# Performance work log

Measured on AMD Instinct MI355X. Metric: run time of the kernel, lower is better.

Reference implementation:

```python
import jax, jax.numpy as jnp
import numpy as np

E = 8       # n_experts
K = 2       # k_experts
D_IN = 1024
D_OUT = 1024
D_EXP = 2048
N = 16384   # tokens (batch*seq, forward requires 2D input)


def setup_inputs() -> dict:
    key = jax.random.key(0)
    ks = jax.random.split(key, 4)
    x = jax.random.normal(ks[0], (N, D_IN), jnp.float32)
    Wg = jax.random.normal(ks[1], (E, D_IN), jnp.float32) * 0.02      # router weight
    bg = jnp.zeros((E,), jnp.float32)                                  # router bias
    W_in = jax.random.normal(ks[2], (E, D_EXP, D_IN), jnp.float32) * 0.02
    b_in = jnp.zeros((E, D_EXP), jnp.float32)                          # w_in_bias_init=0.0
    W_out = jax.random.normal(ks[3], (E, D_OUT, D_EXP), jnp.float32) * 0.02  # bias=False
    return {"x": x, "Wg": Wg, "bg": bg, "W_in": W_in, "b_in": b_in, "W_out": W_out}


def moe_forward(x, Wg, bg, W_in, b_in, W_out):
    # Eval mode: gate jitter / solu jitter / dropouts are training-only no-ops.
    n = x.shape[0]
    # --- routing ---
    logits = x @ Wg.T + bg                                 # [N, E]
    probs = jax.nn.softmax(logits, axis=-1)
    mean_probs = probs.mean(axis=0)                        # [E]
    k_vals, k_idx = jax.lax.top_k(probs, K)                # [N, K]
    k_w = k_vals / k_vals.sum(axis=-1, keepdims=True)      # renormalized gate weights
    counts = jnp.bincount(k_idx.reshape(-1), length=E)     # [E] int
    load_balancing_loss = E * jnp.sum((counts.astype(x.dtype) / n) * mean_probs)
    # --- dispatch + expert w_in (loop over fixed small E; combine with one-hot mask) ---
    sel = jax.nn.one_hot(k_idx, E, dtype=x.dtype)          # [N, K, E]
    h = jnp.zeros((n, K, D_EXP), x.dtype)                  # preacts per (token, slot)
    for e in range(E):
        he = x @ W_in[e].T + b_in[e]                       # [N, D_EXP]
        h = h + sel[:, :, e][..., None] * he[:, None, :]
    # --- SoLU (eval): softmax(preacts) * preacts over hidden dim ---
    acts = jax.nn.softmax(h, axis=-1) * h                  # [N, K, D_EXP]
    # --- expert w_out (no bias) ---
    out = jnp.zeros((n, K, D_OUT), x.dtype)
    for e in range(E):
        oe = jnp.einsum('nkh,oh->nko', acts, W_out[e])
        out = out + sel[:, :, e][..., None] * oe
    # --- weighted combine over the K chosen experts ---
    outputs = (out * k_w[..., None]).sum(axis=1)           # [N, D_OUT]
    return outputs, load_balancing_loss


def reference(x, Wg, bg, W_in, b_in, W_out):
    return moe_forward(x, Wg, bg, W_in, b_in, W_out)
```

## Files before the change

### kernel.cpp

```cpp
#include <hip/hip_runtime.h>
#include <hip/hip_bf16.h>
#include <stdint.h>

#define E_EXP 8
#define NTOK  16384
#define DIN   1024
#define DEXP  2048
#define DOUT  1024
#define NSLOT (NTOK*2)
#define MAXT  264

typedef __attribute__((ext_vector_type(8))) short short8;
typedef __attribute__((ext_vector_type(8))) unsigned short ushort8;
typedef __attribute__((ext_vector_type(4))) unsigned short ushort4v;
typedef __attribute__((ext_vector_type(4))) float f32x4;

__device__ __forceinline__ unsigned short f2bf(float f){
  union { float f; uint32_t u; } v; v.f = f;
  uint32_t r = (v.u + 0x7FFFu + ((v.u >> 16) & 1u)) >> 16;
  return (unsigned short)r;
}
__device__ __forceinline__ float bf2f(unsigned short u){
  union { uint32_t u; float f; } v; v.u = ((uint32_t)u) << 16;
  return v.f;
}

__device__ __forceinline__ void async16(const void* g, void* l){
  __builtin_amdgcn_global_load_lds(
      (const __attribute__((address_space(1))) void*)g,
      (__attribute__((address_space(3))) void*)l, 16, 0, 0);
}

#define VMCNT6() asm volatile("s_waitcnt vmcnt(6)" ::: "memory")
#define VMCNT0() asm volatile("s_waitcnt vmcnt(0)" ::: "memory")
#define BARRIER() do { asm volatile("" ::: "memory"); __builtin_amdgcn_s_barrier(); asm volatile("" ::: "memory"); } while(0)

__global__ __launch_bounds__(256) void cast_bf16(const float* __restrict__ s,
                                                 unsigned short* __restrict__ d, int n){
  int i = (blockIdx.x*256 + threadIdx.x)*8;
  if (i >= n) return;
  float4 a = *(const float4*)(s+i);
  float4 b = *(const float4*)(s+i+4);
  ushort8 o;
  o[0]=f2bf(a.x); o[1]=f2bf(a.y); o[2]=f2bf(a.z); o[3]=f2bf(a.w);
  o[4]=f2bf(b.x); o[5]=f2bf(b.y); o[6]=f2bf(b.z); o[7]=f2bf(b.w);
  *(ushort8*)(d+i) = o;
}

__global__ __launch_bounds__(256) void router(
    const float* __restrict__ x, const float* __restrict__ Wg, const float* __restrict__ bg,
    unsigned short* __restrict__ xb,
    int* __restrict__ eidx, float* __restrict__ gw,
    int* __restrict__ counts, float* __restrict__ probsum)
{
  __shared__ float sWg[E_EXP*DIN];
  __shared__ float sps[E_EXP];
  __shared__ int   scnt[E_EXP];
  const int tid = threadIdx.x;
  for (int i = tid; i < E_EXP*DIN; i += 256) sWg[i] = Wg[i];
  if (tid < E_EXP){ sps[tid]=0.f; scnt[tid]=0; }
  __syncthreads();
  const int lane = tid & 63;
  const int wv   = tid >> 6;
  for (int it = 0; it < 16; ++it){
    const int token = blockIdx.x*64 + wv*16 + it;
    float4 xv[4];
#pragma unroll
    for (int j=0;j<4;++j) xv[j] = *(const float4*)&x[(size_t)token*DIN + j*256 + lane*4];
#pragma unroll
    for (int j=0;j<4;++j){
      ushort4v o;
      o[0]=f2bf(xv[j].x); o[1]=f2bf(xv[j].y); o[2]=f2bf(xv[j].z); o[3]=f2bf(xv[j].w);
      *(ushort4v*)&xb[(size_t)token*DIN + j*256 + lane*4] = o;
    }
    float p[E_EXP];
#pragma unroll
    for (int e2=0;e2<E_EXP;++e2){
      float s = 0.f;
#pragma unroll
      for (int j=0;j<4;++j){
        const float4 w4 = *(const float4*)&sWg[e2*DIN + j*256 + lane*4];
        s += xv[j].x*w4.x + xv[j].y*w4.y + xv[j].z*w4.z + xv[j].w*w4.w;
      }
      p[e2] = s;
    }
#pragma unroll
    for (int d=1; d<64; d<<=1){
#pragma unroll
      for (int e2=0;e2<E_EXP;++e2) p[e2] += __shfl_xor(p[e2], d);
    }
    if (lane == 0){
      float mx = -1e30f;
#pragma unroll
      for (int e2=0;e2<E_EXP;++e2){ p[e2] += bg[e2]; mx = fmaxf(mx, p[e2]); }
      float se = 0.f;
#pragma unroll
      for (int e2=0;e2<E_EXP;++e2){ p[e2] = __expf(p[e2]-mx); se += p[e2]; }
      const float inv = 1.f/se;
#pragma unroll
      for (int e2=0;e2<E_EXP;++e2){ p[e2] *= inv; atomicAdd(&sps[e2], p[e2]); }
      int i1 = 0;
#pragma unroll
      for (int e2=1;e2<E_EXP;++e2) if (p[e2] > p[i1]) i1 = e2;
      int i2 = (i1==0) ? 1 : 0;
#pragma unroll
      for (int e2=0;e2<E_EXP;++e2) if (e2 != i1 && p[e2] > p[i2]) i2 = e2;
      const float v1 = p[i1], v2 = p[i2], s12 = v1 + v2;
      eidx[2*token]   = i1; eidx[2*token+1] = i2;
      gw[2*token]     = v1/s12; gw[2*token+1] = v2/s12;
      atomicAdd(&scnt[i1], 1); atomicAdd(&scnt[i2], 1);
    }
  }
  __syncthreads();
  if (tid < E_EXP){ atomicAdd(&counts[tid], scnt[tid]); atomicAdd(&probsum[tid], sps[tid]); }
}

__global__ void finalize(const int* __restrict__ counts, const float* __restrict__ probsum,
                         float* __restrict__ loss_out, int* __restrict__ offs,
                         int* __restrict__ cursor, int* __restrict__ tile_e,
                         int* __restrict__ tile_row, int* __restrict__ ntiles)
{
  if (threadIdx.x != 0 || blockIdx.x != 0) return;
  int off = 0, nt = 0;
  float loss = 0.f;
  offs[0] = 0;
  for (int e2=0;e2<E_EXP;++e2){
    const int c = counts[e2];
    loss += (float)c * probsum[e2];
    cursor[e2] = 0;
    const int t = (c + 127) >> 7;
    for (int i=0;i<t;++i){ tile_e[nt] = e2; tile_row[nt] = off + i*128; ++nt; }
    off += c;
    offs[e2+1] = off;
  }
  *ntiles = nt;
  *loss_out = loss * (8.f/((float)NTOK*(float)NTOK));
}

__global__ __launch_bounds__(256) void scatter(const int* __restrict__ eidx,
    const int* __restrict__ offs, int* __restrict__ cursor,
    int* __restrict__ ptok, int* __restrict__ inv)
{
  const int t = blockIdx.x*256 + threadIdx.x;
  if (t >= NTOK) return;
#pragma unroll
  for (int s=0;s<2;++s){
    const int e2  = eidx[2*t+s];
    const int pos = offs[e2] + atomicAdd(&cursor[e2], 1);
    ptok[pos] = t;
    inv[2*t+s] = pos;
  }
}

__global__ __launch_bounds__(512, 2) void gemm1(
    const unsigned short* __restrict__ xb,
    const unsigned short* __restrict__ wib,
    const float* __restrict__ b_in,
    unsigned short* __restrict__ H,
    const int* __restrict__ ptok,
    const int* __restrict__ offs,
    const int* __restrict__ tile_e,
    const int* __restrict__ tile_row,
    const int* __restrict__ ntiles)
{
  if ((int)blockIdx.y >= *ntiles) return;
  const int e    = tile_e[blockIdx.y];
  const int row0 = tile_row[blockIdx.y];
  const int seg_end = offs[e+1];
  const int col0 = blockIdx.x * 256;

  __shared__ unsigned short As[2][128*64];
  __shared__ unsigned short Bs[2][256*64];

  const int tid  = threadIdx.x;
  const int lane = tid & 63;
  const int wv   = tid >> 6;
  const int wm   = wv >> 2;
  const int wn   = wv & 3;
  const int srow = tid >> 3;
  const int scol = ((tid & 7) ^ (srow & 7)) * 8;

  const unsigned short* ag[2];
#pragma unroll
  for (int i = 0; i < 2; ++i){
    int g = row0 + i*64 + srow; if (g > NSLOT-1) g = NSLOT-1;
    const int tok = ptok[g];
    ag[i] = xb + (size_t)tok*DIN + scol;
  }
  const unsigned short* bg4[4];
#pragma unroll
  for (int i = 0; i < 4; ++i)
    bg4[i] = wib + ((size_t)e*DEXP + col0 + i*64 + srow)*DIN + scol;
  float bias[4];
#pragma unroll
  for (int n = 0; n < 4; ++n)
    bias[n] = b_in[e*DEXP + col0 + wn*64 + n*16 + (lane&15)];

  f32x4 acc[4][4] = {};
  const int NK = DIN/64;
  int cur = 0;

#pragma unroll
  for (int i = 0; i < 2; ++i) async16(ag[i],  &As[0][(i*64 + wv*8)*64]);
#pragma unroll
  for (int i = 0; i < 4; ++i) async16(bg4[i], &Bs[0][(i*64 + wv*8)*64]);

#pragma unroll 2
  for (int kt = 0; kt < NK; ++kt){
    BARRIER();
    if (kt + 1 < NK){
      const int ko = (kt+1)*64;
#pragma unroll
      for (int i = 0; i < 2; ++i) async16(ag[i]  + ko, &As[cur^1][(i*64 + wv*8)*64]);
#pragma unroll
      for (int i = 0; i < 4; ++i) async16(bg4[i] + ko, &Bs[cur^1][(i*64 + wv*8)*64]);
      VMCNT6();
    } else {
      VMCNT0();
    }
    BARRIER();

    __builtin_amdgcn_s_setprio(1);
#pragma unroll
    for (int kk = 0; kk < 2; ++kk){
      const int ksl = ((kk*4 + (lane>>4)) ^ (lane & 7)) * 8;
      short8 a[4], b[4];
#pragma unroll
      for (int m = 0; m < 4; ++m)
        a[m] = *(const short8*)&As[cur][(wm*64 + m*16 + (lane&15))*64 + ksl];
#pragma unroll
      for (int n = 0; n < 4; ++n)
        b[n] = *(const short8*)&Bs[cur][(wn*64 + n*16 + (lane&15))*64 + ksl];
#pragma unroll
      for (int m = 0; m < 4; ++m)
#pragma unroll
        for (int n = 0; n < 4; ++n)
          acc[m][n] = __builtin_amdgcn_mfma_f32_16x16x32_bf16(a[m], b[n], acc[m][n], 0, 0, 0);
    }
    __builtin_amdgcn_s_setprio(0);
    cur ^= 1;
  }

#pragma unroll
  for (int m = 0; m < 4; ++m){
#pragma unroll
    for (int j = 0; j < 4; ++j){
      const int r = wm*64 + m*16 + (lane>>4)*4 + j;
      const int g = row0 + r;
      if (g < seg_end){
#pragma unroll
        for (int n = 0; n < 4; ++n){
          const int c = col0 + wn*64 + n*16 + (lane&15);
          H[(size_t)g*DEXP + c] = f2bf(acc[m][n][j] + bias[n]);
        }
      }
    }
  }
}

__global__ __launch_bounds__(256) void solu(unsigned short* __restrict__ H){
  const size_t row = blockIdx.x;
  unsigned short* hp = H + row*DEXP;
  const int tid  = threadIdx.x;
  const int lane = tid & 63;
  const int wv   = tid >> 6;
  const short8 hv = *(const short8*)&hp[tid*8];
  float f[8];
#pragma unroll
  for (int j=0;j<8;++j) f[j] = bf2f((unsigned short)hv[j]);
  float mx = f[0];
#pragma unroll
  for (int j=1;j<8;++j) mx = fmaxf(mx, f[j]);
  for (int d=1; d<64; d<<=1) mx = fmaxf(mx, __shfl_xor(mx, d));
  __shared__ float redm[4];
  __shared__ float reds[4];
  if (lane==0) redm[wv] = mx;
  __syncthreads();
  mx = fmaxf(fmaxf(redm[0],redm[1]), fmaxf(redm[2],redm[3]));
  float se = 0.f; float ex[8];
#pragma unroll
  for (int j=0;j<8;++j){ ex[j] = __expf(f[j]-mx); se += ex[j]; }
  for (int d=1; d<64; d<<=1) se += __shfl_xor(se, d);
  if (lane==0) reds[wv] = se;
  __syncthreads();
  se = reds[0]+reds[1]+reds[2]+reds[3];
  const float inv = 1.0f/se;
  ushort8 o;
#pragma unroll
  for (int j=0;j<8;++j) o[j] = f2bf(f[j]*ex[j]*inv);
  *(ushort8*)&hp[tid*8] = o;
}

__global__ __launch_bounds__(512, 2) void gemm2(
    const unsigned short* __restrict__ ACT,
    const unsigned short* __restrict__ wob,
    unsigned short* __restrict__ Oslot,
    const int* __restrict__ offs,
    const int* __restrict__ tile_e,
    const int* __restrict__ tile_row,
    const int* __restrict__ ntiles)
{
  if ((int)blockIdx.y >= *ntiles) return;
  const int e    = tile_e[blockIdx.y];
  const int row0 = tile_row[blockIdx.y];
  const int seg_end = offs[e+1];
  const int col0 = blockIdx.x * 256;

  __shared__ unsigned short As[2][128*64];
  __shared__ unsigned short Bs[2][256*64];

  const int tid  = threadIdx.x;
  const int lane = tid & 63;
  const int wv   = tid >> 6;
  const int wm   = wv >> 2;
  const int wn   = wv & 3;
  const int srow = tid >> 3;
  const int scol = ((tid & 7) ^ (srow & 7)) * 8;

  const unsigned short* ag[2];
#pragma unroll
  for (int i = 0; i < 2; ++i){
    int g = row0 + i*64 + srow; if (g > NSLOT-1) g = NSLOT-1;
    ag[i] = ACT + (size_t)g*DEXP + scol;
  }
  const unsigned short* bg4[4];
#pragma unroll
  for (int i = 0; i < 4; ++i)
    bg4[i] = wob + ((size_t)e*DOUT + col0 + i*64 + srow)*DEXP + scol;

  f32x4 acc[4][4] = {};
  const int NK = DEXP/64;
  int cur = 0;

#pragma unroll
  for (int i = 0; i < 2; ++i) async16(ag[i],  &As[0][(i*64 + wv*8)*64]);
#pragma unroll
  for (int i = 0; i < 4; ++i) async16(bg4[i], &Bs[0][(i*64 + wv*8)*64]);

#pragma unroll 2
  for (int kt = 0; kt < NK; ++kt){
    BARRIER();
    if (kt + 1 < NK){
      const int ko = (kt+1)*64;
#pragma unroll
      for (int i = 0; i < 2; ++i) async16(ag[i]  + ko, &As[cur^1][(i*64 + wv*8)*64]);
#pragma unroll
      for (int i = 0; i < 4; ++i) async16(bg4[i] + ko, &Bs[cur^1][(i*64 + wv*8)*64]);
      VMCNT6();
    } else {
      VMCNT0();
    }
    BARRIER();

    __builtin_amdgcn_s_setprio(1);
#pragma unroll
    for (int kk = 0; kk < 2; ++kk){
      const int ksl = ((kk*4 + (lane>>4)) ^ (lane & 7)) * 8;
      short8 a[4], b[4];
#pragma unroll
      for (int m = 0; m < 4; ++m)
        a[m] = *(const short8*)&As[cur][(wm*64 + m*16 + (lane&15))*64 + ksl];
#pragma unroll
      for (int n = 0; n < 4; ++n)
        b[n] = *(const short8*)&Bs[cur][(wn*64 + n*16 + (lane&15))*64 + ksl];
#pragma unroll
      for (int m = 0; m < 4; ++m)
#pragma unroll
        for (int n = 0; n < 4; ++n)
          acc[m][n] = __builtin_amdgcn_mfma_f32_16x16x32_bf16(a[m], b[n], acc[m][n], 0, 0, 0);
    }
    __builtin_amdgcn_s_setprio(0);
    cur ^= 1;
  }

#pragma unroll
  for (int m = 0; m < 4; ++m){
#pragma unroll
    for (int j = 0; j < 4; ++j){
      const int r = wm*64 + m*16 + (lane>>4)*4 + j;
      const int g = row0 + r;
      if (g < seg_end){
#pragma unroll
        for (int n = 0; n < 4; ++n){
          const int c = col0 + wn*64 + n*16 + (lane&15);
          Oslot[(size_t)g*DOUT + c] = f2bf(acc[m][n][j]);
        }
      }
    }
  }
}

__global__ __launch_bounds__(256) void combine(const unsigned short* __restrict__ Oslot,
    const int* __restrict__ inv, const float* __restrict__ gw, float* __restrict__ out)
{
  const int t    = blockIdx.x*4 + (threadIdx.x >> 6);
  const int lane = threadIdx.x & 63;
  const int p0 = inv[2*t], p1 = inv[2*t+1];
  const float w0 = gw[2*t], w1 = gw[2*t+1];
  const unsigned short* r0 = Oslot + (size_t)p0*DOUT + lane*16;
  const unsigned short* r1 = Oslot + (size_t)p1*DOUT + lane*16;
  ushort8 a0 = *(const ushort8*)r0;
  ushort8 a1 = *(const ushort8*)(r0 + 8);
  ushort8 b0 = *(const ushort8*)r1;
  ushort8 b1 = *(const ushort8*)(r1 + 8);
  float* op = out + (size_t)t*DOUT + lane*16;
  float4 o;
#pragma unroll
  for (int q = 0; q < 2; ++q){
    const ushort8 ua = q ? a1 : a0;
    const ushort8 ub = q ? b1 : b0;
#pragma unroll
    for (int h = 0; h < 2; ++h){
      o.x = w0*bf2f(ua[h*4+0]) + w1*bf2f(ub[h*4+0]);
      o.y = w0*bf2f(ua[h*4+1]) + w1*bf2f(ub[h*4+1]);
      o.z = w0*bf2f(ua[h*4+2]) + w1*bf2f(ub[h*4+2]);
      o.w = w0*bf2f(ua[h*4+3]) + w1*bf2f(ub[h*4+3]);
      *(float4*)(op + q*8 + h*4) = o;
    }
  }
}

extern "C" void kernel_launch(void* const* d_in, const int* in_sizes, int n_in,
                              void* d_out, int out_size, void* d_ws, size_t ws_size,
                              hipStream_t stream)
{
  const float* x     = (const float*)d_in[0];
  const float* Wg    = (const float*)d_in[1];
  const float* bgp   = (const float*)d_in[2];
  const float* W_in  = (const float*)d_in[3];
  const float* b_in  = (const float*)d_in[4];
  const float* W_out = (const float*)d_in[5];
  float* out = (float*)d_out;

  char* base = (char*)d_ws;
  size_t o = 0;
  unsigned short* xb  = (unsigned short*)(base + o); o += (size_t)NTOK*DIN*2;
  unsigned short* wib = (unsigned short*)(base + o); o += (size_t)E_EXP*DEXP*DIN*2;
  unsigned short* wob = (unsigned short*)(base + o); o += (size_t)E_EXP*DOUT*DEXP*2;
  unsigned short* H   = (unsigned short*)(base + o); o += (size_t)NSLOT*DEXP*2;
  unsigned short* Oslot = (unsigned short*)d_ws;
  int*   eidx    = (int*)(base + o);   o += (size_t)NSLOT*4;
  float* gw      = (float*)(base + o); o += (size_t)NSLOT*4;
  int*   ptok    = (int*)(base + o);   o += (size_t)NSLOT*4;
  int*   inv     = (int*)(base + o);   o += (size_t)NSLOT*4;
  int*   counts  = (int*)(base + o);   o += 32;
  float* probsum = (float*)(base + o); o += 32;
  int*   cursor  = (int*)(base + o);   o += 32;
  int*   offs    = (int*)(base + o);   o += 64;
  int*   tile_e  = (int*)(base + o);   o += (size_t)MAXT*4;
  int*   tile_row= (int*)(base + o);   o += (size_t)MAXT*4;
  int*   ntiles  = (int*)(base + o);   o += 64;

  hipMemsetAsync(counts, 0, 96, stream);

  cast_bf16<<<dim3(8192), 256, 0, stream>>>(W_in,  wib, E_EXP*DEXP*DIN);
  cast_bf16<<<dim3(8192), 256, 0, stream>>>(W_out, wob, E_EXP*DOUT*DEXP);

  router<<<dim3(256), 256, 0, stream>>>(x, Wg, bgp, xb, eidx, gw, counts, probsum);
  finalize<<<dim3(1), 64, 0, stream>>>(counts, probsum, out + (size_t)NTOK*DOUT,
                                       offs, cursor, tile_e, tile_row, ntiles);
  scatter<<<dim3(64), 256, 0, stream>>>(eidx, offs, cursor, ptok, inv);

  gemm1<<<dim3(DEXP/256, MAXT), 512, 0, stream>>>(xb, wib, b_in, H, ptok, offs,
                                                  tile_e, tile_row, ntiles);
  solu<<<dim3(NSLOT), 256, 0, stream>>>(H);
  gemm2<<<dim3(DOUT/256, MAXT), 512, 0, stream>>>(H, wob, Oslot, offs,
                                                  tile_e, tile_row, ntiles);
  combine<<<dim3(NTOK/4), 256, 0, stream>>>(Oslot, inv, gw, out);
}
```

Measured before the change: 792.7 us.

## Triple-buffer LDS in both expert GEMMs with one barrier per k-step

Both grouped GEMM kernels move from a double-buffered LDS ring to a three-stage ring with a prefetch distance of two k-tiles. Each iteration now has a single barrier instead of two. The async global-to-LDS loads for the stage two tiles ahead are split into two groups and issued between the two MFMA sub-steps, so memory traffic overlaps compute more evenly. The cost is 1.5x the LDS per block (about 144 KB) and more bookkeeping for the ring indices. The LDS footprint also rules out ever fitting two blocks per CU.

```diff
diff --git a/kernel.cpp b/kernel.cpp
--- a/kernel.cpp
+++ b/kernel.cpp
@@ -9,6 +9,9 @@
 #define DOUT  1024
 #define NSLOT (NTOK*2)
 #define MAXT  264
+
+#define AS_T  (128*64)
+#define BS_T  (256*64)
 
 typedef __attribute__((ext_vector_type(8))) short short8;
 typedef __attribute__((ext_vector_type(8))) unsigned short ushort8;
@@ -169,8 +172,8 @@
   const int seg_end = offs[e+1];
   const int col0 = blockIdx.x * 256;
 
-  __shared__ unsigned short As[2][128*64];
-  __shared__ unsigned short Bs[2][256*64];
+  __shared__ unsigned short As[3*AS_T];
+  __shared__ unsigned short Bs[3*BS_T];
 
   const int tid  = threadIdx.x;
   const int lane = tid & 63;
@@ -198,47 +201,80 @@
 
   f32x4 acc[4][4] = {};
   const int NK = DIN/64;
-  int cur = 0;
-
-#pragma unroll
-  for (int i = 0; i < 2; ++i) async16(ag[i],  &As[0][(i*64 + wv*8)*64]);
-#pragma unroll
-  for (int i = 0; i < 4; ++i) async16(bg4[i], &Bs[0][(i*64 + wv*8)*64]);
-
-#pragma unroll 2
+
+  const unsigned int aL0 = (wv*8)*64, aL1 = (64 + wv*8)*64;
+  const unsigned int bL0 = (wv*8)*64, bL1 = (64+wv*8)*64, bL2 = (128+wv*8)*64, bL3 = (192+wv*8)*64;
+
+#pragma unroll
+  for (int t0 = 0; t0 < 2; ++t0){
+    const int ko = t0*64;
+    async16(ag[0]  + ko, &As[t0*AS_T + aL0]);
+    async16(ag[1]  + ko, &As[t0*AS_T + aL1]);
+    async16(bg4[0] + ko, &Bs[t0*BS_T + bL0]);
+    async16(bg4[1] + ko, &Bs[t0*BS_T + bL1]);
+    async16(bg4[2] + ko, &Bs[t0*BS_T + bL2]);
+    async16(bg4[3] + ko, &Bs[t0*BS_T + bL3]);
+  }
+  VMCNT6();
+  BARRIER();
+
+  int cur = 0, stg = 2;
   for (int kt = 0; kt < NK; ++kt){
-    BARRIER();
-    if (kt + 1 < NK){
-      const int ko = (kt+1)*64;
-#pragma unroll
-      for (int i = 0; i < 2; ++i) async16(ag[i]  + ko, &As[cur^1][(i*64 + wv*8)*64]);
-#pragma unroll
-      for (int i = 0; i < 4; ++i) async16(bg4[i] + ko, &Bs[cur^1][(i*64 + wv*8)*64]);
-      VMCNT6();
-    } else {
-      VMCNT0();
-    }
-    BARRIER();
-
-    __builtin_amdgcn_s_setprio(1);
-#pragma unroll
-    for (int kk = 0; kk < 2; ++kk){
-      const int ksl = ((kk*4 + (lane>>4)) ^ (lane & 7)) * 8;
+    const unsigned short* Ab = &As[cur*AS_T];
+    const unsigned short* Bb = &Bs[cur*BS_T];
+    const int doStage = (kt + 2 < NK);
+    const int ko = (kt+2)*64;
+
+    if (doStage){
+      async16(ag[0]  + ko, &As[stg*AS_T + aL0]);
+      async16(ag[1]  + ko, &As[stg*AS_T + aL1]);
+      async16(bg4[0] + ko, &Bs[stg*BS_T + bL0]);
+    }
+    {
+      const int ksl = (((lane>>4)) ^ (lane & 7)) * 8;
       short8 a[4], b[4];
 #pragma unroll
       for (int m = 0; m < 4; ++m)
-        a[m] = *(const short8*)&As[cur][(wm*64 + m*16 + (lane&15))*64 + ksl];
+        a[m] = *(const short8*)&Ab[(wm*64 + m*16 + (lane&15))*64 + ksl];
 #pragma unroll
       for (int n = 0; n < 4; ++n)
-        b[n] = *(const short8*)&Bs[cur][(wn*64 + n*16 + (lane&15))*64 + ksl];
+        b[n] = *(const short8*)&Bb[(wn*64 + n*16 + (lane&15))*64 + ksl];
+      __builtin_amdgcn_s_setprio(1);
 #pragma unroll
       for (int m = 0; m < 4; ++m)
 #pragma unroll
         for (int n = 0; n < 4; ++n)
           acc[m][n] = __builtin_amdgcn_mfma_f32_16x16x32_bf16(a[m], b[n], acc[m][n], 0, 0, 0);
-    }
-    __builtin_amdgcn_s_setprio(0);
-    cur ^= 1;
+      __builtin_amdgcn_s_setprio(0);
+    }
+
+    if (doStage){
+      async16(bg4[1] + ko, &Bs[stg*BS_T + bL1]);
+      async16(bg4[2] + ko, &Bs[stg*BS_T + bL2]);
+      async16(bg4[3] + ko, &Bs[stg*BS_T + bL3]);
+    }
+    {
+      const int ksl = ((4 + (lane>>4)) ^ (lane & 7)) * 8;
+      short8 a[4], b[4];
+#pragma unroll
+      for (int m = 0; m < 4; ++m)
+        a[m] = *(const short8*)&Ab[(wm*64 + m*16 + (lane&15))*64 + ksl];
+#pragma unroll
+      for (int n = 0; n < 4; ++n)
+        b[n] = *(const short8*)&Bb[(wn*64 + n*16 + (lane&15))*64 + ksl];
+      __builtin_amdgcn_s_setprio(1);
+#pragma unroll
+      for (int m = 0; m < 4; ++m)
+#pragma unroll
+        for (int n = 0; n < 4; ++n)
+          acc[m][n] = __builtin_amdgcn_mfma_f32_16x16x32_bf16(a[m], b[n], acc[m][n], 0, 0, 0);
+      __builtin_amdgcn_s_setprio(0);
+    }
+
+    if (doStage) { VMCNT6(); } else { VMCNT0(); }
+    BARRIER();
+    cur = (cur == 2) ? 0 : cur + 1;
+    stg = (stg == 2) ? 0 : stg + 1;
   }
 
 #pragma unroll
@@ -306,8 +342,8 @@
   const int seg_end = offs[e+1];
   const int col0 = blockIdx.x * 256;
 
-  __shared__ unsigned short As[2][128*64];
-  __shared__ unsigned short Bs[2][256*64];
+  __shared__ unsigned short As[3*AS_T];
+  __shared__ unsigned short Bs[3*BS_T];
 
   const int tid  = threadIdx.x;
   const int lane = tid & 63;
@@ -330,47 +366,80 @@
 
   f32x4 acc[4][4] = {};
   const int NK = DEXP/64;
-  int cur = 0;
-
-#pragma unroll
-  for (int i = 0; i < 2; ++i) async16(ag[i],  &As[0][(i*64 + wv*8)*64]);
-#pragma unroll
-  for (int i = 0; i < 4; ++i) async16(bg4[i], &Bs[0][(i*64 + wv*8)*64]);
-
-#pragma unroll 2
+
+  const unsigned int aL0 = (wv*8)*64, aL1 = (64 + wv*8)*64;
+  const unsigned int bL0 = (wv*8)*64, bL1 = (64+wv*8)*64, bL2 = (128+wv*8)*64, bL3 = (192+wv*8)*64;
+
+#pragma unroll
+  for (int t0 = 0; t0 < 2; ++t0){
+    const int ko = t0*64;
+    async16(ag[0]  + ko, &As[t0*AS_T + aL0]);
+    async16(ag[1]  + ko, &As[t0*AS_T + aL1]);
+    async16(bg4[0] + ko, &Bs[t0*BS_T + bL0]);
+    async16(bg4[1] + ko, &Bs[t0*BS_T + bL1]);
+    async16(bg4[2] + ko, &Bs[t0*BS_T + bL2]);
+    async16(bg4[3] + ko, &Bs[t0*BS_T + bL3]);
+  }
+  VMCNT6();
+  BARRIER();
+
+  int cur = 0, stg = 2;
   for (int kt = 0; kt < NK; ++kt){
-    BARRIER();
-    if (kt + 1 < NK){
-      const int ko = (kt+1)*64;
-#pragma unroll
-      for (int i = 0; i < 2; ++i) async16(ag[i]  + ko, &As[cur^1][(i*64 + wv*8)*64]);
-#pragma unroll
-      for (int i = 0; i < 4; ++i) async16(bg4[i] + ko, &Bs[cur^1][(i*64 + wv*8)*64]);
-      VMCNT6();
-    } else {
-      VMCNT0();
-    }
-    BARRIER();
-
-    __builtin_amdgcn_s_setprio(1);
-#pragma unroll
-    for (int kk = 0; kk < 2; ++kk){
-      const int ksl = ((kk*4 + (lane>>4)) ^ (lane & 7)) * 8;
+    const unsigned short* Ab = &As[cur*AS_T];
+    const unsigned short* Bb = &Bs[cur*BS_T];
+    const int doStage = (kt + 2 < NK);
+    const int ko = (kt+2)*64;
+
+    if (doStage){
+      async16(ag[0]  + ko, &As[stg*AS_T + aL0]);
+      async16(ag[1]  + ko, &As[stg*AS_T + aL1]);
+      async16(bg4[0] + ko, &Bs[stg*BS_T + bL0]);
+    }
+    {
+      const int ksl = (((lane>>4)) ^ (lane & 7)) * 8;
       short8 a[4], b[4];
 #pragma unroll
       for (int m = 0; m < 4; ++m)
-        a[m] = *(const short8*)&As[cur][(wm*64 + m*16 + (lane&15))*64 + ksl];
+        a[m] = *(const short8*)&Ab[(wm*64 + m*16 + (lane&15))*64 + ksl];
 #pragma unroll
       for (int n = 0; n < 4; ++n)
-        b[n] = *(const short8*)&Bs[cur][(wn*64 + n*16 + (lane&15))*64 + ksl];
+        b[n] = *(const short8*)&Bb[(wn*64 + n*16 + (lane&15))*64 + ksl];
+      __builtin_amdgcn_s_setprio(1);
 #pragma unroll
       for (int m = 0; m < 4; ++m)
 #pragma unroll
         for (int n = 0; n < 4; ++n)
           acc[m][n] = __builtin_amdgcn_mfma_f32_16x16x32_bf16(a[m], b[n], acc[m][n], 0, 0, 0);
-    }
-    __builtin_amdgcn_s_setprio(0);
-    cur ^= 1;
+      __builtin_amdgcn_s_setprio(0);
+    }
+
+    if (doStage){
+      async16(bg4[1] + ko, &Bs[stg*BS_T + bL1]);
+      async16(bg4[2] + ko, &Bs[stg*BS_T + bL2]);
+      async16(bg4[3] + ko, &Bs[stg*BS_T + bL3]);
+    }
+    {
+      const int ksl = ((4 + (lane>>4)) ^ (lane & 7)) * 8;
+      short8 a[4], b[4];
+#pragma unroll
+      for (int m = 0; m < 4; ++m)
+        a[m] = *(const short8*)&Ab[(wm*64 + m*16 + (lane&15))*64 + ksl];
+#pragma unroll
+      for (int n = 0; n < 4; ++n)
+        b[n] = *(const short8*)&Bb[(wn*64 + n*16 + (lane&15))*64 + ksl];
+      __builtin_amdgcn_s_setprio(1);
+#pragma unroll
+      for (int m = 0; m < 4; ++m)
+#pragma unroll
+        for (int n = 0; n < 4; ++n)
+          acc[m][n] = __builtin_amdgcn_mfma_f32_16x16x32_bf16(a[m], b[n], acc[m][n], 0, 0, 0);
+      __builtin_amdgcn_s_setprio(0);
+    }
+
+    if (doStage) { VMCNT6(); } else { VMCNT0(); }
+    BARRIER();
+    cur = (cur == 2) ? 0 : cur + 1;
+    stg = (stg == 2) ? 0 : stg + 1;
   }
 
 #pragma unroll
```

Measured after the change: 908.3 us. 1.15x slower.
